# Optimization experiments

Hardware: AMD Instinct MI355X
Metric: run time of the kernel (lower is better)

The kernel has to match this reference:

```python
import jax, jax.numpy as jnp
import numpy as np

H = 4096          # hidden_size
NH = 32           # num query heads
NKV = 8           # num kv heads
HD = H // NH      # head_dim = 128
GROUPS = NH // NKV
ROPE_BASE = 100000.0
B, S = 1, 2048


def setup_inputs() -> dict:
    key = jax.random.key(0)
    k1, k2, k3 = jax.random.split(key, 3)
    hidden_states = jax.random.normal(k1, (B, S, H), dtype=jnp.float32)
    position_ids = jnp.broadcast_to(jnp.arange(S, dtype=jnp.int32), (B, S))
    op_size = NH * HD + 2 * NKV * HD  # 6144
    w_qkv = jax.random.normal(k2, (op_size, H), dtype=jnp.float32) * 0.02
    w_o = jax.random.normal(k3, (H, H), dtype=jnp.float32) * 0.02
    return {"hidden_states": hidden_states, "position_ids": position_ids,
            "w_qkv": w_qkv, "w_o": w_o}


def _rotate_half(x):
    x1, x2 = x[..., : HD // 2], x[..., HD // 2 :]
    return jnp.concatenate((-x2, x1), axis=-1)


def _rope_cos_sin(position_ids, dtype):
    # inv_freq: [HD/2]
    inv_freq = 1.0 / (ROPE_BASE ** (jnp.arange(0, HD, 2, dtype=jnp.float32) / HD))
    freqs = position_ids.astype(jnp.float32)[..., None] * inv_freq  # [B,S,HD/2]
    emb = jnp.concatenate((freqs, freqs), axis=-1)                  # [B,S,HD]
    return jnp.cos(emb).astype(dtype), jnp.sin(emb).astype(dtype)


def reference(hidden_states, position_ids, w_qkv, w_o):
    b, s, _ = hidden_states.shape
    qkv = jnp.einsum('bsh,oh->bso', hidden_states, w_qkv)
    q_end = NH * HD
    k_end = q_end + NKV * HD
    q = qkv[..., :q_end].reshape(b, s, NH, HD)
    k = qkv[..., q_end:k_end].reshape(b, s, NKV, HD)
    v = qkv[..., k_end:].reshape(b, s, NKV, HD)

    cos, sin = _rope_cos_sin(position_ids, hidden_states.dtype)  # [B,S,HD]
    cos, sin = cos[:, :, None, :], sin[:, :, None, :]            # broadcast over heads
    q = q * cos + _rotate_half(q) * sin
    k = k * cos + _rotate_half(k) * sin

    # GQA: repeat kv heads
    k = jnp.repeat(k, GROUPS, axis=2)  # [B,S,NH,HD]
    v = jnp.repeat(v, GROUPS, axis=2)

    scale = 1.0 / jnp.sqrt(jnp.asarray(HD, dtype=q.dtype))
    scores = jnp.einsum('bqhd,bkhd->bhqk', q, k) * scale  # [B,NH,S,S]
    causal = jnp.tril(jnp.ones((s, s), dtype=bool))
    scores = jnp.where(causal[None, None], scores, jnp.finfo(scores.dtype).min)
    probs = jax.nn.softmax(scores, axis=-1)
    attn = jnp.einsum('bhqk,bkhd->bqhd', probs, v).reshape(b, s, H)
    return jnp.einsum('bsh,oh->bso', attn, w_o)
```

## Files before the change

kernel.cpp:

```cpp
#include <hip/hip_runtime.h>

#define SEQ     2048
#define HDIM    4096
#define NHEADS  32
#define NKVH    8
#define HEADD   128
#define QKV_LD  6144
#define K_OFF   4096
#define V_OFF   5120

typedef __bf16 bf16x8 __attribute__((ext_vector_type(8)));
typedef float  f32x4  __attribute__((ext_vector_type(4)));

__device__ inline float bf2f(unsigned short u) {
  return __uint_as_float(((unsigned int)u) << 16);
}
__device__ inline unsigned short f2bf(float f) {
  unsigned int u = __float_as_uint(f);
  u += 0x7fff + ((u >> 16) & 1);
  return (unsigned short)(u >> 16);
}
__device__ inline unsigned int pack2bf(float a, float b) {
  return (unsigned int)f2bf(a) | ((unsigned int)f2bf(b) << 16);
}

__global__ __launch_bounds__(256) void cvt_bf16(
    const float* __restrict__ s, unsigned short* __restrict__ d, int n8) {
  int i = blockIdx.x * 256 + threadIdx.x;
  int stride = gridDim.x * 256;
  for (; i < n8; i += stride) {
    const float* p = s + (size_t)i * 8;
    float4 x = *(const float4*)p;
    float4 y = *(const float4*)(p + 4);
    uint4 pk;
    pk.x = pack2bf(x.x, x.y);
    pk.y = pack2bf(x.z, x.w);
    pk.z = pack2bf(y.x, y.y);
    pk.w = pack2bf(y.z, y.w);
    *(uint4*)(d + (size_t)i * 8) = pk;
  }
}

template<int A_BF16, int B_BF16, int C_F32>
__global__ __launch_bounds__(256, 2) void gemm_bt(
    const void* __restrict__ Av,
    const void* __restrict__ Bv,
    void* __restrict__ Cv,
    int K, int lda, int ldb, int ldc) {
  __shared__ __align__(16) unsigned short sA[128][64];
  __shared__ __align__(16) unsigned short sB[128][64];

  const int t    = threadIdx.x;
  const int wave = t >> 6;
  const int lane = t & 63;
  const int lrow = lane & 15;
  const int kgrp = lane >> 4;
  const int wm   = (wave >> 1) * 64;
  const int wn   = (wave & 1) * 64;
  const int m0   = blockIdx.x * 128;
  const int n0   = blockIdx.y * 128;

  f32x4 acc[4][4];
  #pragma unroll
  for (int i = 0; i < 4; ++i)
    #pragma unroll
    for (int j = 0; j < 4; ++j)
      #pragma unroll
      for (int e = 0; e < 4; ++e) acc[i][j][e] = 0.f;

  for (int k0 = 0; k0 < K; k0 += 64) {
    __syncthreads();
    if constexpr (A_BF16) {
      #pragma unroll
      for (int c = 0; c < 4; ++c) {
        int chunk = wave * 4 + c;
        int row   = chunk * 8 + (lane >> 3);
        int cg    = (lane & 7) ^ ((lane >> 3) & 7);
        __builtin_amdgcn_global_load_lds(
            (const __attribute__((address_space(1))) unsigned int*)
                ((const unsigned short*)Av + (size_t)(m0 + row) * lda + k0 + cg * 8),
            (__attribute__((address_space(3))) unsigned int*)&sA[chunk * 8][0],
            16, 0, 0);
      }
    } else {
      #pragma unroll
      for (int r = 0; r < 4; ++r) {
        int row = r * 32 + (t >> 3);
        int cg  = t & 7;
        const float* p = (const float*)Av + (size_t)(m0 + row) * lda + k0 + cg * 8;
        float4 x = *(const float4*)p;
        float4 y = *(const float4*)(p + 4);
        uint4 pk;
        pk.x = pack2bf(x.x, x.y);
        pk.y = pack2bf(x.z, x.w);
        pk.z = pack2bf(y.x, y.y);
        pk.w = pack2bf(y.z, y.w);
        *(uint4*)&sA[row][(cg ^ (row & 7)) * 8] = pk;
      }
    }
    if constexpr (B_BF16) {
      #pragma unroll
      for (int c = 0; c < 4; ++c) {
        int chunk = wave * 4 + c;
        int row   = chunk * 8 + (lane >> 3);
        int cg    = (lane & 7) ^ ((lane >> 3) & 7);
        __builtin_amdgcn_global_load_lds(
            (const __attribute__((address_space(1))) unsigned int*)
                ((const unsigned short*)Bv + (size_t)(n0 + row) * ldb + k0 + cg * 8),
            (__attribute__((address_space(3))) unsigned int*)&sB[chunk * 8][0],
            16, 0, 0);
      }
    } else {
      #pragma unroll
      for (int r = 0; r < 4; ++r) {
        int row = r * 32 + (t >> 3);
        int cg  = t & 7;
        const float* p = (const float*)Bv + (size_t)(n0 + row) * ldb + k0 + cg * 8;
        float4 x = *(const float4*)p;
        float4 y = *(const float4*)(p + 4);
        uint4 pk;
        pk.x = pack2bf(x.x, x.y);
        pk.y = pack2bf(x.z, x.w);
        pk.z = pack2bf(y.x, y.y);
        pk.w = pack2bf(y.z, y.w);
        *(uint4*)&sB[row][(cg ^ (row & 7)) * 8] = pk;
      }
    }
    __syncthreads();

    #pragma unroll
    for (int ks = 0; ks < 2; ++ks) {
      bf16x8 af[4], bfm[4];
      #pragma unroll
      for (int i = 0; i < 4; ++i)
        af[i] = *(const bf16x8*)&sA[wm + i*16 + lrow][((ks*4 + kgrp) ^ (lrow & 7)) * 8];
      #pragma unroll
      for (int j = 0; j < 4; ++j)
        bfm[j] = *(const bf16x8*)&sB[wn + j*16 + lrow][((ks*4 + kgrp) ^ (lrow & 7)) * 8];
      #pragma unroll
      for (int i = 0; i < 4; ++i)
        #pragma unroll
        for (int j = 0; j < 4; ++j)
          acc[i][j] = __builtin_amdgcn_mfma_f32_16x16x32_bf16(af[i], bfm[j], acc[i][j], 0, 0, 0);
    }
  }

  #pragma unroll
  for (int i = 0; i < 4; ++i) {
    #pragma unroll
    for (int r = 0; r < 4; ++r) {
      int row = m0 + wm + i*16 + kgrp*4 + r;
      #pragma unroll
      for (int j = 0; j < 4; ++j) {
        int col = n0 + wn + j*16 + lrow;
        if constexpr (C_F32)
          ((float*)Cv)[(size_t)row * ldc + col] = acc[i][j][r];
        else
          ((unsigned short*)Cv)[(size_t)row * ldc + col] = f2bf(acc[i][j][r]);
      }
    }
  }
}

__global__ __launch_bounds__(256) void rope_kernel(
    unsigned short* __restrict__ qkv, const int* __restrict__ pos) {
  int tid  = blockIdx.x * 256 + threadIdx.x;
  int d    = tid & 63;
  int rh   = tid >> 6;
  int head = rh % 40;
  int s    = rh / 40;
  if (s >= SEQ) return;
  unsigned short* p = qkv + (size_t)s * QKV_LD + head * 128 + d;
  float x1 = bf2f(p[0]);
  float x2 = bf2f(p[64]);
  float inv = __expf((float)d * -0.17988946039016608f);
  float ang = (float)pos[s] * inv;
  float sn, c;
  sincosf(ang, &sn, &c);
  p[0]  = f2bf(x1 * c - x2 * sn);
  p[64] = f2bf(x2 * c + x1 * sn);
}

__global__ __launch_bounds__(256) void transpose_v(
    const unsigned short* __restrict__ qkv, unsigned short* __restrict__ vT) {
  __shared__ unsigned short tile[64][72];
  const int t  = threadIdx.x;
  const int s0 = blockIdx.x * 64;
  const int c0 = blockIdx.y * 64;
  const int r  = t >> 3;
  const int cg = (t & 7) * 8;
  #pragma unroll
  for (int rr = 0; rr < 2; ++rr) {
    int row = rr * 32 + r;
    *(uint4*)&tile[row][cg] =
        *(const uint4*)(qkv + (size_t)(s0 + row) * QKV_LD + V_OFF + c0 + cg);
  }
  __syncthreads();
  #pragma unroll
  for (int rr = 0; rr < 2; ++rr) {
    int c = rr * 32 + r;
    unsigned short v[8];
    #pragma unroll
    for (int j = 0; j < 8; ++j) v[j] = tile[cg + j][c];
    *(uint4*)(vT + (size_t)(c0 + c) * SEQ + s0 + cg) = *(uint4*)v;
  }
}

__device__ __forceinline__ void qk_softmax_tile(
    const bf16x8* qf, const unsigned short (*sK)[128],
    unsigned short (*sP)[72],
    f32x4* of, float* m_i, float* l_i,
    int lane, int wave, int dq) {
  const int lrow = lane & 15;
  const int kgrp = lane >> 4;
  f32x4 st[4];
  #pragma unroll
  for (int tn = 0; tn < 4; ++tn)
    #pragma unroll
    for (int e = 0; e < 4; ++e) st[tn][e] = 0.f;
  #pragma unroll
  for (int ks = 0; ks < 4; ++ks) {
    #pragma unroll
    for (int tn = 0; tn < 4; ++tn) {
      int cgr = ks * 4 + kgrp;
      const bf16x8 kb = *(const bf16x8*)
          &sK[tn*16 + lrow][((cgr & 8) | ((cgr & 7) ^ (lrow & 7))) * 8];
      st[tn] = __builtin_amdgcn_mfma_f32_16x16x32_bf16(qf[ks], kb, st[tn], 0, 0, 0);
    }
  }
  const float scale2 = 0.12751743f;
  float mrow[4] = {-1e30f, -1e30f, -1e30f, -1e30f};
  #pragma unroll
  for (int tn = 0; tn < 4; ++tn) {
    #pragma unroll
    for (int r = 0; r < 4; ++r) {
      float s = st[tn][r] * scale2;
      if (tn*16 + lrow > dq + r) s = -1e30f;
      st[tn][r] = s;
      mrow[r] = fmaxf(mrow[r], s);
    }
  }
  #pragma unroll
  for (int r = 0; r < 4; ++r)
    #pragma unroll
    for (int off = 1; off < 16; off <<= 1)
      mrow[r] = fmaxf(mrow[r], __shfl_xor(mrow[r], off, 16));
  float alpha[4];
  #pragma unroll
  for (int r = 0; r < 4; ++r) {
    float mnew = fmaxf(m_i[r], mrow[r]);
    alpha[r] = exp2f(m_i[r] - mnew);
    m_i[r] = mnew;
  }
  float rsum[4] = {0.f, 0.f, 0.f, 0.f};
  #pragma unroll
  for (int tn = 0; tn < 4; ++tn)
    #pragma unroll
    for (int r = 0; r < 4; ++r) {
      float pr = exp2f(st[tn][r] - m_i[r]);
      rsum[r] += pr;
      sP[wave*16 + kgrp*4 + r][tn*16 + lrow] = f2bf(pr);
    }
  #pragma unroll
  for (int r = 0; r < 4; ++r) {
    #pragma unroll
    for (int off = 1; off < 16; off <<= 1)
      rsum[r] += __shfl_xor(rsum[r], off, 16);
    l_i[r] = l_i[r] * alpha[r] + rsum[r];
  }
  #pragma unroll
  for (int tt = 0; tt < 8; ++tt)
    #pragma unroll
    for (int r = 0; r < 4; ++r)
      of[tt][r] *= alpha[r];
}

__device__ __forceinline__ void pv_tile(
    const unsigned short (*sP)[72], const unsigned short (*sVt)[64],
    f32x4* of, int lane, int wave) {
  const int lrow = lane & 15;
  const int kgrp = lane >> 4;
  #pragma unroll
  for (int ks = 0; ks < 2; ++ks) {
    const bf16x8 pa = *(const bf16x8*)&sP[wave*16 + lrow][ks*32 + kgrp*8];
    #pragma unroll
    for (int tt = 0; tt < 8; ++tt) {
      int cgr = ks * 4 + kgrp;
      const bf16x8 vb = *(const bf16x8*)
          &sVt[tt*16 + lrow][(cgr ^ (lrow & 7)) * 8];
      of[tt] = __builtin_amdgcn_mfma_f32_16x16x32_bf16(pa, vb, of[tt], 0, 0, 0);
    }
  }
}

__global__ __launch_bounds__(256, 2) void attn_fwd2(
    unsigned short* __restrict__ qkv, const unsigned short* __restrict__ vT) {
  __shared__ __align__(16) unsigned short sK[64][128];
  __shared__ __align__(16) unsigned short sVt[128][64];
  __shared__ __align__(16) unsigned short sP[128][72];

  const int t    = threadIdx.x;
  const int wave = t >> 6;
  const int lane = t & 63;
  const int lrow = lane & 15;
  const int kgrp = lane >> 4;
  const int p    = blockIdx.x;
  const int h    = blockIdx.y;
  const int kvh  = h >> 2;
  const int qLo  = p * 64;
  const int qHi  = (31 - p) * 64;
  const int nTiles = 32 - p;
  const int nDual  = p + 1;

  bf16x8 qfH[4], qfL[4];
  {
    const unsigned short* qr =
        qkv + (size_t)(qHi + wave*16 + lrow) * QKV_LD + h * HEADD;
    #pragma unroll
    for (int ks = 0; ks < 4; ++ks) qfH[ks] = *(const bf16x8*)(qr + ks*32 + kgrp*8);
    qr = qkv + (size_t)(qLo + wave*16 + lrow) * QKV_LD + h * HEADD;
    #pragma unroll
    for (int ks = 0; ks < 4; ++ks) qfL[ks] = *(const bf16x8*)(qr + ks*32 + kgrp*8);
  }

  f32x4 ofH[8], ofL[8];
  float mH[4], lH[4], mL[4], lL[4];
  #pragma unroll
  for (int tt = 0; tt < 8; ++tt)
    #pragma unroll
    for (int e = 0; e < 4; ++e) { ofH[tt][e] = 0.f; ofL[tt][e] = 0.f; }
  #pragma unroll
  for (int r = 0; r < 4; ++r) { mH[r] = -1e30f; lH[r] = 0.f; mL[r] = -1e30f; lL[r] = 0.f; }

  for (int kt = 0; kt < nTiles; ++kt) {
    const int k0 = kt * 64;
    __syncthreads();
    #pragma unroll
    for (int c = 0; c < 4; ++c) {
      int cc   = wave * 4 + c;
      int grow = cc * 4 + (lane >> 4);
      int slot = lane & 15;
      int cg   = (slot & 8) | ((slot & 7) ^ (grow & 7));
      __builtin_amdgcn_global_load_lds(
          (const __attribute__((address_space(1))) unsigned int*)
              (qkv + (size_t)(k0 + grow) * QKV_LD + K_OFF + kvh*HEADD + cg*8),
          (__attribute__((address_space(3))) unsigned int*)&sK[cc*4][0],
          16, 0, 0);
    }
    #pragma unroll
    for (int c = 0; c < 4; ++c) {
      int cc   = wave * 4 + c;
      int grow = cc * 8 + (lane >> 3);
      int slot = lane & 7;
      int cg   = slot ^ (grow & 7);
      __builtin_amdgcn_global_load_lds(
          (const __attribute__((address_space(1))) unsigned int*)
              (vT + (size_t)(kvh*HEADD + grow) * SEQ + k0 + cg*8),
          (__attribute__((address_space(3))) unsigned int*)&sVt[cc*8][0],
          16, 0, 0);
    }
    __syncthreads();

    const bool dual = (kt < nDual);
    qk_softmax_tile(qfH, sK, &sP[0],  ofH, mH, lH, lane, wave,
                    qHi + wave*16 + kgrp*4 - k0);
    if (dual)
      qk_softmax_tile(qfL, sK, &sP[64], ofL, mL, lL, lane, wave,
                      qLo + wave*16 + kgrp*4 - k0);
    __syncthreads();
    pv_tile(&sP[0], sVt, ofH, lane, wave);
    if (dual) pv_tile(&sP[64], sVt, ofL, lane, wave);
  }

  #pragma unroll
  for (int r = 0; r < 4; ++r) {
    float invH = 1.f / lH[r];
    float invL = 1.f / lL[r];
    int rowH = qHi + wave*16 + kgrp*4 + r;
    int rowL = qLo + wave*16 + kgrp*4 + r;
    #pragma unroll
    for (int tt = 0; tt < 8; ++tt) {
      qkv[(size_t)rowH * QKV_LD + h*HEADD + tt*16 + lrow] = f2bf(ofH[tt][r] * invH);
      qkv[(size_t)rowL * QKV_LD + h*HEADD + tt*16 + lrow] = f2bf(ofL[tt][r] * invL);
    }
  }
}

__global__ __launch_bounds__(256, 2) void attn_fwd(
    unsigned short* __restrict__ qkv) {
  __shared__ __align__(16) unsigned short sK[64][136];
  __shared__ __align__(16) unsigned short sVt[128][72];
  __shared__ __align__(16) unsigned short sP[64][72];

  const int t    = threadIdx.x;
  const int wave = t >> 6;
  const int lane = t & 63;
  const int lrow = lane & 15;
  const int kgrp = lane >> 4;
  const int q0   = blockIdx.x * 64;
  const int h    = blockIdx.y;
  const int kvh  = h >> 2;

  bf16x8 qf[4];
  {
    const unsigned short* qrow =
        qkv + (size_t)(q0 + wave*16 + lrow) * QKV_LD + h * HEADD;
    #pragma unroll
    for (int ks = 0; ks < 4; ++ks)
      qf[ks] = *(const bf16x8*)(qrow + ks*32 + kgrp*8);
  }

  f32x4 of[8];
  #pragma unroll
  for (int tt = 0; tt < 8; ++tt)
    #pragma unroll
    for (int e = 0; e < 4; ++e) of[tt][e] = 0.f;
  float m_i[4], l_i[4];
  #pragma unroll
  for (int r = 0; r < 4; ++r) { m_i[r] = -1e30f; l_i[r] = 0.f; }

  const float scale = 0.08838834764831845f;

  for (int k0 = 0; k0 <= q0; k0 += 64) {
    __syncthreads();
    {
      int krow = t >> 4;
      int kcol = (t & 15) * 8;
      #pragma unroll
      for (int r = 0; r < 4; ++r)
        *(uint4*)&sK[r*16 + krow][kcol] =
            *(const uint4*)(qkv + (size_t)(k0 + r*16 + krow) * QKV_LD + K_OFF + kvh*HEADD + kcol);
      int vrow = t & 15;
      int vcol = (t >> 4) * 8;
      #pragma unroll
      for (int r = 0; r < 4; ++r) {
        uint4 v = *(const uint4*)(qkv + (size_t)(k0 + r*16 + vrow) * QKV_LD + V_OFF + kvh*HEADD + vcol);
        const unsigned short* pv = (const unsigned short*)&v;
        #pragma unroll
        for (int j = 0; j < 8; ++j)
          sVt[vcol + j][r*16 + vrow] = pv[j];
      }
    }
    __syncthreads();

    f32x4 st[4];
    #pragma unroll
    for (int tn = 0; tn < 4; ++tn)
      #pragma unroll
      for (int e = 0; e < 4; ++e) st[tn][e] = 0.f;
    #pragma unroll
    for (int ks = 0; ks < 4; ++ks)
      #pragma unroll
      for (int tn = 0; tn < 4; ++tn) {
        bf16x8 kb = *(const bf16x8*)&sK[tn*16 + lrow][ks*32 + kgrp*8];
        st[tn] = __builtin_amdgcn_mfma_f32_16x16x32_bf16(qf[ks], kb, st[tn], 0, 0, 0);
      }

    float mrow[4];
    #pragma unroll
    for (int r = 0; r < 4; ++r) mrow[r] = -1e30f;
    const int qrow_base = q0 + wave*16 + kgrp*4;
    #pragma unroll
    for (int tn = 0; tn < 4; ++tn) {
      int kcol = k0 + tn*16 + lrow;
      #pragma unroll
      for (int r = 0; r < 4; ++r) {
        float s = st[tn][r] * scale;
        if (kcol > qrow_base + r) s = -1e30f;
        st[tn][r] = s;
        mrow[r] = fmaxf(mrow[r], s);
      }
    }
    #pragma unroll
    for (int r = 0; r < 4; ++r)
      #pragma unroll
      for (int off = 1; off < 16; off <<= 1)
        mrow[r] = fmaxf(mrow[r], __shfl_xor(mrow[r], off, 16));

    float alpha[4];
    #pragma unroll
    for (int r = 0; r < 4; ++r) {
      float mnew = fmaxf(m_i[r], mrow[r]);
      alpha[r] = __expf(m_i[r] - mnew);
      m_i[r] = mnew;
    }

    float rsum[4] = {0.f, 0.f, 0.f, 0.f};
    #pragma unroll
    for (int tn = 0; tn < 4; ++tn)
      #pragma unroll
      for (int r = 0; r < 4; ++r) {
        float pr = __expf(st[tn][r] - m_i[r]);
        rsum[r] += pr;
        sP[wave*16 + kgrp*4 + r][tn*16 + lrow] = f2bf(pr);
      }
    #pragma unroll
    for (int r = 0; r < 4; ++r) {
      #pragma unroll
      for (int off = 1; off < 16; off <<= 1)
        rsum[r] += __shfl_xor(rsum[r], off, 16);
      l_i[r] = l_i[r] * alpha[r] + rsum[r];
    }
    #pragma unroll
    for (int tt = 0; tt < 8; ++tt)
      #pragma unroll
      for (int r = 0; r < 4; ++r)
        of[tt][r] *= alpha[r];

    __syncthreads();

    #pragma unroll
    for (int ks = 0; ks < 2; ++ks) {
      bf16x8 pa = *(const bf16x8*)&sP[wave*16 + lrow][ks*32 + kgrp*8];
      #pragma unroll
      for (int tt = 0; tt < 8; ++tt) {
        bf16x8 vb = *(const bf16x8*)&sVt[tt*16 + lrow][ks*32 + kgrp*8];
        of[tt] = __builtin_amdgcn_mfma_f32_16x16x32_bf16(pa, vb, of[tt], 0, 0, 0);
      }
    }
  }

  #pragma unroll
  for (int r = 0; r < 4; ++r) {
    int row = q0 + wave*16 + kgrp*4 + r;
    float inv = 1.f / l_i[r];
    #pragma unroll
    for (int tt = 0; tt < 8; ++tt)
      qkv[(size_t)row * QKV_LD + h*HEADD + tt*16 + lrow] = f2bf(of[tt][r] * inv);
  }
}

extern "C" void kernel_launch(void* const* d_in, const int* in_sizes, int n_in,
                              void* d_out, int out_size, void* d_ws, size_t ws_size,
                              hipStream_t stream) {
  const float* hs    = (const float*)d_in[0];
  const int*   pos   = (const int*)d_in[1];
  const float* w_qkv = (const float*)d_in[2];
  const float* w_o   = (const float*)d_in[3];
  float*       out   = (float*)d_out;

  const size_t N_QKV  = (size_t)SEQ * QKV_LD;
  const size_t N_HS   = (size_t)SEQ * HDIM;
  const size_t N_WQKV = (size_t)QKV_LD * HDIM;
  const size_t N_WO   = (size_t)HDIM * HDIM;

  unsigned short* qkv = (unsigned short*)d_ws;

  const size_t full_ws = (N_QKV + N_HS + N_WQKV + N_WO) * 2;

  if (ws_size >= full_ws) {
    unsigned short* hs_b   = qkv + N_QKV;
    unsigned short* wqkv_b = hs_b + N_HS;
    unsigned short* wo_b   = wqkv_b + N_WQKV;
    unsigned short* vT     = hs_b;

    cvt_bf16<<<2048, 256, 0, stream>>>(hs,    hs_b,   (int)(N_HS   / 8));
    cvt_bf16<<<2048, 256, 0, stream>>>(w_qkv, wqkv_b, (int)(N_WQKV / 8));
    cvt_bf16<<<2048, 256, 0, stream>>>(w_o,   wo_b,   (int)(N_WO   / 8));

    gemm_bt<1, 1, 0><<<dim3(SEQ/128, QKV_LD/128), 256, 0, stream>>>(
        hs_b, wqkv_b, qkv, HDIM, HDIM, HDIM, QKV_LD);
    rope_kernel<<<(SEQ * 40 * 64) / 256, 256, 0, stream>>>(qkv, pos);
    transpose_v<<<dim3(SEQ/64, (NKVH*HEADD)/64), 256, 0, stream>>>(qkv, vT);
    attn_fwd2<<<dim3(16, NHEADS), 256, 0, stream>>>(qkv, vT);
    gemm_bt<1, 1, 1><<<dim3(SEQ/128, HDIM/128), 256, 0, stream>>>(
        qkv, wo_b, out, HDIM, QKV_LD, HDIM, HDIM);
  } else {
    gemm_bt<0, 0, 0><<<dim3(SEQ/128, QKV_LD/128), 256, 0, stream>>>(
        hs, w_qkv, qkv, HDIM, HDIM, HDIM, QKV_LD);
    rope_kernel<<<(SEQ * 40 * 64) / 256, 256, 0, stream>>>(qkv, pos);
    attn_fwd<<<dim3(SEQ/64, NHEADS), 256, 0, stream>>>(qkv);
    gemm_bt<1, 0, 1><<<dim3(SEQ/128, HDIM/128), 256, 0, stream>>>(
        qkv, w_o, out, HDIM, QKV_LD, HDIM, HDIM);
  }
}
```

Baseline: 537.1 us.

## Fuse conversions and rope/transpose launches, fold softmax scale into Q, skip off-diagonal masking

Merges the three fp32→bf16 conversions into one launch, and fuses RoPE with the V transpose into one kernel. RoPE now computes sin/cos once per (position, dim) and reuses it across all 40 Q/K heads instead of recomputing per head. In the attention kernel the softmax scale is folded into the Q fragments once at load time, and causal masking is applied only on diagonal tiles. This cuts launch overhead, redundant transcendental math and per-element ALU work, at the cost of an extra bf16 rounding on the pre-scaled Q.

```diff
diff --git a/kernel.cpp b/kernel.cpp
--- a/kernel.cpp
+++ b/kernel.cpp
@@ -24,12 +24,17 @@
   return (unsigned int)f2bf(a) | ((unsigned int)f2bf(b) << 16);
 }
 
-__global__ __launch_bounds__(256) void cvt_bf16(
-    const float* __restrict__ s, unsigned short* __restrict__ d, int n8) {
-  int i = blockIdx.x * 256 + threadIdx.x;
-  int stride = gridDim.x * 256;
-  for (; i < n8; i += stride) {
-    const float* p = s + (size_t)i * 8;
+__global__ __launch_bounds__(256) void cvt_all(
+    const float* __restrict__ s0, const float* __restrict__ s1,
+    const float* __restrict__ s2, unsigned short* __restrict__ d,
+    int n0_8, int n1_8, int n2_8) {
+  const int total = n0_8 + n1_8 + n2_8;
+  for (int i = blockIdx.x * 256 + threadIdx.x; i < total; i += gridDim.x * 256) {
+    const float* s; int off;
+    if (i < n0_8)              { s = s0; off = i; }
+    else if (i < n0_8 + n1_8)  { s = s1; off = i - n0_8; }
+    else                       { s = s2; off = i - n0_8 - n1_8; }
+    const float* p = s + (size_t)off * 8;
     float4 x = *(const float4*)p;
     float4 y = *(const float4*)(p + 4);
     uint4 pk;
@@ -162,55 +167,65 @@
   }
 }
 
-__global__ __launch_bounds__(256) void rope_kernel(
-    unsigned short* __restrict__ qkv, const int* __restrict__ pos) {
-  int tid  = blockIdx.x * 256 + threadIdx.x;
-  int d    = tid & 63;
-  int rh   = tid >> 6;
-  int head = rh % 40;
-  int s    = rh / 40;
-  if (s >= SEQ) return;
-  unsigned short* p = qkv + (size_t)s * QKV_LD + head * 128 + d;
-  float x1 = bf2f(p[0]);
-  float x2 = bf2f(p[64]);
-  float inv = __expf((float)d * -0.17988946039016608f);
-  float ang = (float)pos[s] * inv;
-  float sn, c;
-  sincosf(ang, &sn, &c);
-  p[0]  = f2bf(x1 * c - x2 * sn);
-  p[64] = f2bf(x2 * c + x1 * sn);
-}
-
-__global__ __launch_bounds__(256) void transpose_v(
-    const unsigned short* __restrict__ qkv, unsigned short* __restrict__ vT) {
+__global__ __launch_bounds__(256) void rope_transpose(
+    unsigned short* __restrict__ qkv, const int* __restrict__ pos,
+    unsigned short* __restrict__ vT) {
   __shared__ unsigned short tile[64][72];
-  const int t  = threadIdx.x;
-  const int s0 = blockIdx.x * 64;
-  const int c0 = blockIdx.y * 64;
-  const int r  = t >> 3;
-  const int cg = (t & 7) * 8;
-  #pragma unroll
-  for (int rr = 0; rr < 2; ++rr) {
-    int row = rr * 32 + r;
-    *(uint4*)&tile[row][cg] =
-        *(const uint4*)(qkv + (size_t)(s0 + row) * QKV_LD + V_OFF + c0 + cg);
-  }
-  __syncthreads();
-  #pragma unroll
-  for (int rr = 0; rr < 2; ++rr) {
-    int c = rr * 32 + r;
-    unsigned short v[8];
-    #pragma unroll
-    for (int j = 0; j < 8; ++j) v[j] = tile[cg + j][c];
-    *(uint4*)(vT + (size_t)(c0 + c) * SEQ + s0 + cg) = *(uint4*)v;
-  }
+  int b = blockIdx.x;
+  if (b < 512) {
+    int tid = b * 256 + threadIdx.x;
+    int d   = tid & 63;
+    int s   = tid >> 6;
+    float inv = __expf((float)d * -0.17988946039016608f);
+    float ang = (float)pos[s] * inv;
+    float sn, c;
+    sincosf(ang, &sn, &c);
+    unsigned short* base = qkv + (size_t)s * QKV_LD + d;
+    #pragma unroll 4
+    for (int head = 0; head < 40; ++head) {
+      unsigned short* p = base + head * 128;
+      float x1 = bf2f(p[0]);
+      float x2 = bf2f(p[64]);
+      p[0]  = f2bf(x1 * c - x2 * sn);
+      p[64] = f2bf(x2 * c + x1 * sn);
+    }
+  } else {
+    b -= 512;
+    const int t  = threadIdx.x;
+    const int s0 = (b & 31) * 64;
+    const int c0 = (b >> 5) * 64;
+    const int r  = t >> 3;
+    const int cg = (t & 7) * 8;
+    #pragma unroll
+    for (int rr = 0; rr < 2; ++rr) {
+      int row = rr * 32 + r;
+      *(uint4*)&tile[row][cg] =
+          *(const uint4*)(qkv + (size_t)(s0 + row) * QKV_LD + V_OFF + c0 + cg);
+    }
+    __syncthreads();
+    #pragma unroll
+    for (int rr = 0; rr < 2; ++rr) {
+      int c = rr * 32 + r;
+      unsigned short v[8];
+      #pragma unroll
+      for (int j = 0; j < 8; ++j) v[j] = tile[cg + j][c];
+      *(uint4*)(vT + (size_t)(c0 + c) * SEQ + s0 + cg) = *(uint4*)v;
+    }
+  }
+}
+
+__device__ inline bf16x8 scale_frag(bf16x8 v, float s) {
+  bf16x8 r;
+  #pragma unroll
+  for (int j = 0; j < 8; ++j) r[j] = (__bf16)((float)v[j] * s);
+  return r;
 }
 
 __device__ __forceinline__ void qk_softmax_tile(
     const bf16x8* qf, const unsigned short (*sK)[128],
     unsigned short (*sP)[72],
     f32x4* of, float* m_i, float* l_i,
-    int lane, int wave, int dq) {
+    int lane, int wave, int dq, bool diag) {
   const int lrow = lane & 15;
   const int kgrp = lane >> 4;
   f32x4 st[4];
@@ -228,17 +243,23 @@
       st[tn] = __builtin_amdgcn_mfma_f32_16x16x32_bf16(qf[ks], kb, st[tn], 0, 0, 0);
     }
   }
-  const float scale2 = 0.12751743f;
   float mrow[4] = {-1e30f, -1e30f, -1e30f, -1e30f};
-  #pragma unroll
-  for (int tn = 0; tn < 4; ++tn) {
-    #pragma unroll
-    for (int r = 0; r < 4; ++r) {
-      float s = st[tn][r] * scale2;
-      if (tn*16 + lrow > dq + r) s = -1e30f;
-      st[tn][r] = s;
-      mrow[r] = fmaxf(mrow[r], s);
-    }
+  if (diag) {
+    #pragma unroll
+    for (int tn = 0; tn < 4; ++tn)
+      #pragma unroll
+      for (int r = 0; r < 4; ++r) {
+        float s = st[tn][r];
+        if (tn*16 + lrow > dq + r) s = -1e30f;
+        st[tn][r] = s;
+        mrow[r] = fmaxf(mrow[r], s);
+      }
+  } else {
+    #pragma unroll
+    for (int tn = 0; tn < 4; ++tn)
+      #pragma unroll
+      for (int r = 0; r < 4; ++r)
+        mrow[r] = fmaxf(mrow[r], st[tn][r]);
   }
   #pragma unroll
   for (int r = 0; r < 4; ++r)
@@ -312,15 +333,18 @@
   const int nTiles = 32 - p;
   const int nDual  = p + 1;
 
+  const float scale2 = 0.12751743f;
   bf16x8 qfH[4], qfL[4];
   {
     const unsigned short* qr =
         qkv + (size_t)(qHi + wave*16 + lrow) * QKV_LD + h * HEADD;
     #pragma unroll
-    for (int ks = 0; ks < 4; ++ks) qfH[ks] = *(const bf16x8*)(qr + ks*32 + kgrp*8);
+    for (int ks = 0; ks < 4; ++ks)
+      qfH[ks] = scale_frag(*(const bf16x8*)(qr + ks*32 + kgrp*8), scale2);
     qr = qkv + (size_t)(qLo + wave*16 + lrow) * QKV_LD + h * HEADD;
     #pragma unroll
-    for (int ks = 0; ks < 4; ++ks) qfL[ks] = *(const bf16x8*)(qr + ks*32 + kgrp*8);
+    for (int ks = 0; ks < 4; ++ks)
+      qfL[ks] = scale_frag(*(const bf16x8*)(qr + ks*32 + kgrp*8), scale2);
   }
 
   f32x4 ofH[8], ofL[8];
@@ -363,10 +387,10 @@
 
     const bool dual = (kt < nDual);
     qk_softmax_tile(qfH, sK, &sP[0],  ofH, mH, lH, lane, wave,
-                    qHi + wave*16 + kgrp*4 - k0);
+                    qHi + wave*16 + kgrp*4 - k0, k0 == qHi);
     if (dual)
       qk_softmax_tile(qfL, sK, &sP[64], ofL, mL, lL, lane, wave,
-                      qLo + wave*16 + kgrp*4 - k0);
+                      qLo + wave*16 + kgrp*4 - k0, k0 == qLo);
     __syncthreads();
     pv_tile(&sP[0], sVt, ofH, lane, wave);
     if (dual) pv_tile(&sP[64], sVt, ofL, lane, wave);
@@ -383,6 +407,27 @@
       qkv[(size_t)rowH * QKV_LD + h*HEADD + tt*16 + lrow] = f2bf(ofH[tt][r] * invH);
       qkv[(size_t)rowL * QKV_LD + h*HEADD + tt*16 + lrow] = f2bf(ofL[tt][r] * invL);
     }
+  }
+}
+
+__global__ __launch_bounds__(256) void rope_kernel(
+    unsigned short* __restrict__ qkv, const int* __restrict__ pos) {
+  int tid  = blockIdx.x * 256 + threadIdx.x;
+  int d    = tid & 63;
+  int s    = tid >> 6;
+  if (s >= SEQ) return;
+  float inv = __expf((float)d * -0.17988946039016608f);
+  float ang = (float)pos[s] * inv;
+  float sn, c;
+  sincosf(ang, &sn, &c);
+  unsigned short* base = qkv + (size_t)s * QKV_LD + d;
+  #pragma unroll 4
+  for (int head = 0; head < 40; ++head) {
+    unsigned short* p = base + head * 128;
+    float x1 = bf2f(p[0]);
+    float x2 = bf2f(p[64]);
+    p[0]  = f2bf(x1 * c - x2 * sn);
+    p[64] = f2bf(x2 * c + x1 * sn);
   }
 }
 
@@ -554,21 +599,19 @@
     unsigned short* wo_b   = wqkv_b + N_WQKV;
     unsigned short* vT     = hs_b;
 
-    cvt_bf16<<<2048, 256, 0, stream>>>(hs,    hs_b,   (int)(N_HS   / 8));
-    cvt_bf16<<<2048, 256, 0, stream>>>(w_qkv, wqkv_b, (int)(N_WQKV / 8));
-    cvt_bf16<<<2048, 256, 0, stream>>>(w_o,   wo_b,   (int)(N_WO   / 8));
-
+    cvt_all<<<2048, 256, 0, stream>>>(hs, w_qkv, w_o, hs_b,
+                                      (int)(N_HS / 8), (int)(N_WQKV / 8),
+                                      (int)(N_WO / 8));
     gemm_bt<1, 1, 0><<<dim3(SEQ/128, QKV_LD/128), 256, 0, stream>>>(
         hs_b, wqkv_b, qkv, HDIM, HDIM, HDIM, QKV_LD);
-    rope_kernel<<<(SEQ * 40 * 64) / 256, 256, 0, stream>>>(qkv, pos);
-    transpose_v<<<dim3(SEQ/64, (NKVH*HEADD)/64), 256, 0, stream>>>(qkv, vT);
+    rope_transpose<<<1024, 256, 0, stream>>>(qkv, pos, vT);
     attn_fwd2<<<dim3(16, NHEADS), 256, 0, stream>>>(qkv, vT);
     gemm_bt<1, 1, 1><<<dim3(SEQ/128, HDIM/128), 256, 0, stream>>>(
         qkv, wo_b, out, HDIM, QKV_LD, HDIM, HDIM);
   } else {
     gemm_bt<0, 0, 0><<<dim3(SEQ/128, QKV_LD/128), 256, 0, stream>>>(
         hs, w_qkv, qkv, HDIM, HDIM, HDIM, QKV_LD);
-    rope_kernel<<<(SEQ * 40 * 64) / 256, 256, 0, stream>>>(qkv, pos);
+    rope_kernel<<<SEQ * 64 / 256, 256, 0, stream>>>(qkv, pos);
     attn_fwd<<<dim3(SEQ/64, NHEADS), 256, 0, stream>>>(qkv);
     gemm_bt<1, 0, 1><<<dim3(SEQ/128, HDIM/128), 256, 0, stream>>>(
         qkv, w_o, out, HDIM, QKV_LD, HDIM, HDIM);
```

Result: no change. 529.2 us (-1.5%).
